# Kernel optimization log

Measured on AMD Instinct MI355X. Metric: run time of the kernel, lower is better.

## Reference

```python
import jax, jax.numpy as jnp
import numpy as np

B, S, D = 16, 2048, 1024
FF = 4 * D
ST, EN = 0, 512          # target_dims['start'], target_dims['end']
DT = EN - ST             # intervened subspace dim


def setup_inputs() -> dict:
    key = jax.random.key(0)
    k = jax.random.split(key, 6)
    hidden_states = jax.random.normal(k[0], (B, S, D), dtype=jnp.float32)
    eot_indices = jax.random.randint(k[1], (B,), 0, S)
    scale = 0.02
    W1 = jax.random.normal(k[2], (D, FF), dtype=jnp.float32) * scale
    W2 = jax.random.normal(k[3], (FF, D), dtype=jnp.float32) * scale
    W_rot = jax.random.normal(k[4], (DT, DT), dtype=jnp.float32) * scale
    W_inv = jax.random.normal(k[5], (DT, DT), dtype=jnp.float32) * scale
    return {"hidden_states": hidden_states, "W1": W1, "W2": W2,
            "W_rot": W_rot, "W_inv": W_inv, "eot_indices": eot_indices}


def reference(hidden_states, W1, W2, W_rot, W_inv, eot_indices):
    # layers[0]: transformer FFN block (stand-in for the wrapped encoder layer)
    h = jax.nn.gelu(hidden_states @ W1) @ W2          # [B, S, D]
    b = jnp.arange(h.shape[0])
    # LinearLayer branch: gather per-example eot row, slice target subspace
    rows = h[b, eot_indices]                          # [B, D]
    target = rows[:, ST:EN]                           # [B, DT]
    # LinearLayer -> InverseLinearLayer: rotate then un-rotate the subspace
    intervention = (target @ W_rot) @ W_inv           # [B, DT]
    # scatter/replace back into the flattened hidden states (vectorized form
    # of the per-example flatten/slice/cat/stack loop in the original code)
    new_rows = rows.at[:, ST:EN].set(intervention)    # [B, D]
    reps = h.at[b, eot_indices].set(new_rows)         # [B, S, D]
    return reps
```

## Files before the change

kernel.cpp:

```cpp
#include <hip/hip_runtime.h>
#include <hip/hip_bf16.h>
#include <stdint.h>

#define B_SZ  16
#define S_SZ  2048
#define D_SZ  1024
#define FF_SZ 4096
#define DT_SZ 512

typedef __bf16 bf16x8 __attribute__((ext_vector_type(8)));
typedef float  f32x4  __attribute__((ext_vector_type(4)));
typedef short  short8 __attribute__((ext_vector_type(8)));

__device__ __forceinline__ short f2bf(float x) {
    union { float f; uint32_t u; } v; v.f = x;
    uint32_t r = (v.u + 0x7fffu + ((v.u >> 16) & 1u)) >> 16;
    return (short)(uint16_t)r;
}

__global__ void cast_x_kernel(const float* __restrict__ src, short* __restrict__ dst, int n8) {
    int i = blockIdx.x * 256 + threadIdx.x;
    if (i >= n8) return;
    const float4* s4 = reinterpret_cast<const float4*>(src);
    float4 a = s4[2 * i], b = s4[2 * i + 1];
    short8 v;
    v[0] = f2bf(a.x); v[1] = f2bf(a.y); v[2] = f2bf(a.z); v[3] = f2bf(a.w);
    v[4] = f2bf(b.x); v[5] = f2bf(b.y); v[6] = f2bf(b.z); v[7] = f2bf(b.w);
    reinterpret_cast<short8*>(dst)[i] = v;
}

__global__ void transpose_cast_kernel(const float* __restrict__ src, short* __restrict__ dst,
                                      int R, int C) {
    __shared__ float tile[32][33];
    int c0 = blockIdx.x * 32, r0 = blockIdx.y * 32;
    int tx = threadIdx.x, ty = threadIdx.y;
#pragma unroll
    for (int i = 0; i < 32; i += 8)
        tile[ty + i][tx] = src[(size_t)(r0 + ty + i) * C + (c0 + tx)];
    __syncthreads();
#pragma unroll
    for (int i = 0; i < 32; i += 8)
        dst[(size_t)(c0 + ty + i) * R + (r0 + tx)] = f2bf(tile[tx][ty + i]);
}


#define GLOAD(srcp, dstofs)                                                   \
    __builtin_amdgcn_global_load_lds(                                         \
        (__attribute__((address_space(1))) void*)(srcp),                      \
        (__attribute__((address_space(3))) void*)(ldsb + (dstofs)), 16, 0, 0)

template <bool GELU_BF16>
__global__ __launch_bounds__(256, 4)
void gemm128_kernel(const short* __restrict__ A, const short* __restrict__ Bt,
                    void* __restrict__ Cout, int M, int N, int K) {
    __shared__ char lds[32768];
    char* ldsb = &lds[0];

    const int tid = threadIdx.x;
    const int w   = tid >> 6;
    const int l   = tid & 63;
    const int wm  = w >> 1;
    const int wn  = w & 1;
    const int kq  = l >> 4;
    const int l15 = l & 15;

    const int nwg = gridDim.x;
    int swzw = blockIdx.x;
    if ((nwg & 7) == 0) swzw = (swzw & 7) * (nwg >> 3) + (swzw >> 3);
    const int NB = N >> 7;
    const int bm = swzw / NB, bn = swzw % NB;
    const int m0 = bm << 7, n0 = bn << 7;

    int offA[4], offB[4];
#pragma unroll
    for (int mi = 0; mi < 4; ++mi) {
        const int r = wm * 64 + mi * 16 + l15;
        offA[mi] = r * 128 + ((kq ^ (r & 7)) << 4);
    }
#pragma unroll
    for (int ni = 0; ni < 4; ++ni) {
        const int r = wn * 64 + ni * 16 + l15;
        offB[ni] = 16384 + r * 128 + ((kq ^ (r & 7)) << 4);
    }

    const short *gA[4], *gB[4];
#pragma unroll
    for (int j = 0; j < 4; ++j) {
        const int X = j * 4096 + tid * 16;
        const int P = X ^ (((X >> 7) & 7) << 4);
        const int r = P >> 7, c = (P & 127) >> 1;
        gA[j] = A  + (size_t)(m0 + r) * K + c;
        gB[j] = Bt + (size_t)(n0 + r) * K + c;
    }

    f32x4 acc[4][4];
#pragma unroll
    for (int mi = 0; mi < 4; ++mi)
#pragma unroll
        for (int ni = 0; ni < 4; ++ni)
            acc[mi][ni] = (f32x4){0.f, 0.f, 0.f, 0.f};

    const int NT = K >> 6;

    for (int t = 0; t < NT; ++t) {
        __syncthreads();
#pragma unroll
        for (int j = 0; j < 4; ++j) {
            GLOAD(gA[j] + (size_t)t * 64,         j * 4096 + tid * 16);
            GLOAD(gB[j] + (size_t)t * 64, 16384 + j * 4096 + tid * 16);
        }
        __syncthreads();
#pragma unroll
        for (int ks = 0; ks < 2; ++ks) {
            bf16x8 a[4], b[4];
#pragma unroll
            for (int mi = 0; mi < 4; ++mi)
                a[mi] = *reinterpret_cast<const bf16x8*>(ldsb + (offA[mi] ^ (ks << 6)));
#pragma unroll
            for (int ni = 0; ni < 4; ++ni)
                b[ni] = *reinterpret_cast<const bf16x8*>(ldsb + (offB[ni] ^ (ks << 6)));
#pragma unroll
            for (int mi = 0; mi < 4; ++mi)
#pragma unroll
                for (int ni = 0; ni < 4; ++ni)
                    acc[mi][ni] = __builtin_amdgcn_mfma_f32_16x16x32_bf16(
                        a[mi], b[ni], acc[mi][ni], 0, 0, 0);
        }
    }

    const int row_base = m0 + wm * 64 + kq * 4;
    const int col_base = n0 + wn * 64 + l15;
    if constexpr (GELU_BF16) {
        short* C = reinterpret_cast<short*>(Cout);
#pragma unroll
        for (int mi = 0; mi < 4; ++mi)
#pragma unroll
            for (int r = 0; r < 4; ++r) {
                const size_t ro = (size_t)(row_base + mi * 16 + r) * N;
#pragma unroll
                for (int ni = 0; ni < 4; ++ni) {
                    float x = acc[mi][ni][r];
                    float u = 0.7978845608028654f * (x + 0.044715f * x * x * x);
                    float g = x / (1.f + __expf(-2.f * u));
                    C[ro + col_base + ni * 16] = f2bf(g);
                }
            }
    } else {
        float* C = reinterpret_cast<float*>(Cout);
#pragma unroll
        for (int mi = 0; mi < 4; ++mi)
#pragma unroll
            for (int r = 0; r < 4; ++r) {
                const size_t ro = (size_t)(row_base + mi * 16 + r) * N;
#pragma unroll
                for (int ni = 0; ni < 4; ++ni)
                    C[ro + col_base + ni * 16] = acc[mi][ni][r];
            }
    }
}

__global__ void intervention_kernel(const float* __restrict__ Wrot, const float* __restrict__ Winv,
                                    const int* __restrict__ eot, float* __restrict__ out) {
    __shared__ float tgt[DT_SZ];
    __shared__ float tmp[DT_SZ];
    const int b = blockIdx.x;
    const int j = threadIdx.x;
    float* row = out + ((size_t)b * S_SZ + eot[b]) * D_SZ;
    tgt[j] = row[j];
    __syncthreads();
    float s = 0.f;
#pragma unroll 8
    for (int i = 0; i < DT_SZ; ++i) s = fmaf(tgt[i], Wrot[(size_t)i * DT_SZ + j], s);
    tmp[j] = s;
    __syncthreads();
    float s2 = 0.f;
#pragma unroll 8
    for (int i = 0; i < DT_SZ; ++i) s2 = fmaf(tmp[i], Winv[(size_t)i * DT_SZ + j], s2);
    row[j] = s2;
}

extern "C" void kernel_launch(void* const* d_in, const int* in_sizes, int n_in,
                              void* d_out, int out_size, void* d_ws, size_t ws_size,
                              hipStream_t stream) {
    const float* hidden = (const float*)d_in[0];
    const float* W1     = (const float*)d_in[1];
    const float* W2     = (const float*)d_in[2];
    const float* Wrot   = (const float*)d_in[3];
    const float* Winv   = (const float*)d_in[4];
    const int*   eot    = (const int*)d_in[5];
    float* out = (float*)d_out;

    const int M = B_SZ * S_SZ;

    short* W1t = (short*)d_ws;
    short* W2t = W1t + (size_t)FF_SZ * D_SZ;
    short* Xbf = W2t + (size_t)FF_SZ * D_SZ;
    const size_t fixed_bytes = 2ull * (size_t)FF_SZ * D_SZ * sizeof(short);
    const size_t per_row = (size_t)D_SZ * 2 + (size_t)FF_SZ * 2;
    size_t rem = ws_size > fixed_bytes ? ws_size - fixed_bytes : 0;
    int Mc = (int)(rem / per_row);
    Mc = (Mc / 512) * 512;
    if (Mc < 512) Mc = 512;
    if (Mc > M) Mc = M;
    short* C1 = Xbf + (size_t)Mc * D_SZ;

    transpose_cast_kernel<<<dim3(FF_SZ / 32, D_SZ / 32), dim3(32, 8), 0, stream>>>(W1, W1t, D_SZ, FF_SZ);
    transpose_cast_kernel<<<dim3(D_SZ / 32, FF_SZ / 32), dim3(32, 8), 0, stream>>>(W2, W2t, FF_SZ, D_SZ);

    for (int ms = 0; ms < M; ms += Mc) {
        const int mc = (M - ms < Mc) ? (M - ms) : Mc;
        const int n8 = mc * D_SZ / 8;
        cast_x_kernel<<<(n8 + 255) / 256, 256, 0, stream>>>(hidden + (size_t)ms * D_SZ, Xbf, n8);
        gemm128_kernel<true ><<<dim3((mc / 128) * (FF_SZ / 128)), 256, 0, stream>>>(
            Xbf, W1t, C1, mc, FF_SZ, D_SZ);
        gemm128_kernel<false><<<dim3((mc / 128) * (D_SZ / 128)), 256, 0, stream>>>(
            C1, W2t, out + (size_t)ms * D_SZ, mc, D_SZ, FF_SZ);
    }
    intervention_kernel<<<B_SZ, DT_SZ, 0, stream>>>(Wrot, Winv, eot, out);
}
```

Before: 731.8 us.

## Double-buffer GEMM LDS tiles with BK=32 and prefetch next K-slice

```diff
diff --git a/kernel.cpp b/kernel.cpp
--- a/kernel.cpp
+++ b/kernel.cpp
@@ -49,6 +49,32 @@
         (__attribute__((address_space(1))) void*)(srcp),                      \
         (__attribute__((address_space(3))) void*)(ldsb + (dstofs)), 16, 0, 0)
 
+#define STAGE(S, T) do {                                                                    \
+    GLOAD(gA[0] + (size_t)(T) * 32, (S) * 16384 +         tid * 16);                        \
+    GLOAD(gA[1] + (size_t)(T) * 32, (S) * 16384 +  4096 + tid * 16);                        \
+    GLOAD(gB[0] + (size_t)(T) * 32, (S) * 16384 +  8192 + tid * 16);                        \
+    GLOAD(gB[1] + (size_t)(T) * 32, (S) * 16384 + 12288 + tid * 16);                        \
+} while (0)
+
+#define TILE(S, T, STG) do {                                                                \
+    asm volatile("s_waitcnt vmcnt(0)" ::: "memory");                                        \
+    __builtin_amdgcn_s_barrier();                                                           \
+    if (STG) STAGE((S) ^ 1, (T) + 1);                                                       \
+    bf16x8 a[4], b[4];                                                                      \
+    _Pragma("unroll")                                                                       \
+    for (int mi = 0; mi < 4; ++mi)                                                          \
+        a[mi] = *reinterpret_cast<const bf16x8*>(ldsb + (S) * 16384 + offA[mi]);            \
+    _Pragma("unroll")                                                                       \
+    for (int ni = 0; ni < 4; ++ni)                                                          \
+        b[ni] = *reinterpret_cast<const bf16x8*>(ldsb + (S) * 16384 + offB[ni]);            \
+    _Pragma("unroll")                                                                       \
+    for (int mi = 0; mi < 4; ++mi)                                                          \
+        _Pragma("unroll")                                                                   \
+        for (int ni = 0; ni < 4; ++ni)                                                      \
+            acc[mi][ni] = __builtin_amdgcn_mfma_f32_16x16x32_bf16(                          \
+                a[mi], b[ni], acc[mi][ni], 0, 0, 0);                                        \
+} while (0)
+
 template <bool GELU_BF16>
 __global__ __launch_bounds__(256, 4)
 void gemm128_kernel(const short* __restrict__ A, const short* __restrict__ Bt,
@@ -75,20 +101,20 @@
 #pragma unroll
     for (int mi = 0; mi < 4; ++mi) {
         const int r = wm * 64 + mi * 16 + l15;
-        offA[mi] = r * 128 + ((kq ^ (r & 7)) << 4);
+        offA[mi] = (r * 64 + kq * 16) ^ (((r >> 1) & 7) << 4);
     }
 #pragma unroll
     for (int ni = 0; ni < 4; ++ni) {
         const int r = wn * 64 + ni * 16 + l15;
-        offB[ni] = 16384 + r * 128 + ((kq ^ (r & 7)) << 4);
-    }
-
-    const short *gA[4], *gB[4];
-#pragma unroll
-    for (int j = 0; j < 4; ++j) {
+        offB[ni] = 8192 + ((r * 64 + kq * 16) ^ (((r >> 1) & 7) << 4));
+    }
+
+    const short *gA[2], *gB[2];
+#pragma unroll
+    for (int j = 0; j < 2; ++j) {
         const int X = j * 4096 + tid * 16;
         const int P = X ^ (((X >> 7) & 7) << 4);
-        const int r = P >> 7, c = (P & 127) >> 1;
+        const int r = P >> 6, c = (P & 63) >> 1;
         gA[j] = A  + (size_t)(m0 + r) * K + c;
         gB[j] = Bt + (size_t)(n0 + r) * K + c;
     }
@@ -100,33 +126,17 @@
         for (int ni = 0; ni < 4; ++ni)
             acc[mi][ni] = (f32x4){0.f, 0.f, 0.f, 0.f};
 
-    const int NT = K >> 6;
-
-    for (int t = 0; t < NT; ++t) {
-        __syncthreads();
-#pragma unroll
-        for (int j = 0; j < 4; ++j) {
-            GLOAD(gA[j] + (size_t)t * 64,         j * 4096 + tid * 16);
-            GLOAD(gB[j] + (size_t)t * 64, 16384 + j * 4096 + tid * 16);
-        }
-        __syncthreads();
-#pragma unroll
-        for (int ks = 0; ks < 2; ++ks) {
-            bf16x8 a[4], b[4];
-#pragma unroll
-            for (int mi = 0; mi < 4; ++mi)
-                a[mi] = *reinterpret_cast<const bf16x8*>(ldsb + (offA[mi] ^ (ks << 6)));
-#pragma unroll
-            for (int ni = 0; ni < 4; ++ni)
-                b[ni] = *reinterpret_cast<const bf16x8*>(ldsb + (offB[ni] ^ (ks << 6)));
-#pragma unroll
-            for (int mi = 0; mi < 4; ++mi)
-#pragma unroll
-                for (int ni = 0; ni < 4; ++ni)
-                    acc[mi][ni] = __builtin_amdgcn_mfma_f32_16x16x32_bf16(
-                        a[mi], b[ni], acc[mi][ni], 0, 0, 0);
-        }
-    }
+    const int NT = K >> 5;
+
+    STAGE(0, 0);
+
+    int t = 0;
+    for (; t + 2 < NT; t += 2) {
+        TILE(0, t, 1);
+        TILE(1, t + 1, 1);
+    }
+    TILE(0, t, 1);
+    TILE(1, t + 1, 0);
 
     const int row_base = m0 + wm * 64 + kq * 4;
     const int col_base = n0 + wn * 64 + l15;
```

Result: slower. 804.8 us (+10.0%).
